# Kernel tuning notes

Measured on AMD Instinct MI355X. Metric: run time of the kernel, lower is better.

Reference implementation:

```python
import jax, jax.numpy as jnp
import numpy as np

B, D, H, DH, L = 2, 1024, 16, 64, 4
FF = 4 * D
COUNTS = (512, 256, 128, 64, 16)  # seq, local_seq, scattering, expression, fusion
EPS = 1e-5


def layer_norm(x, gamma):
    mu = jnp.mean(x, axis=-1, keepdims=True)
    var = jnp.mean((x - mu) ** 2, axis=-1, keepdims=True)
    return (x - mu) * jax.lax.rsqrt(var + EPS) * gamma


def build_zorro_mask(counts):
    # faithful to the torch code, including the `|` / `==` precedence quirk:
    # zorro_mask_fusion = (zorro_mask | tf) == FUSION(4)
    types = jnp.concatenate([jnp.full((c,), i, dtype=jnp.int32) for i, c in enumerate(counts)])
    tf, tt = types[:, None], types[None, :]
    m0 = tf == tt
    fusion_rows = (m0.astype(jnp.int32) | tf) == 4
    mask = m0 | fusion_rows
    S = int(sum(counts))
    nf = counts[4]
    exp_rows = (types == 3)[:, None]
    col_ok = (jnp.arange(S) < (S - nf))[None, :]
    return mask | (exp_rows & col_ok)


def setup_inputs() -> dict:
    key = jax.random.key(0)
    ks = jax.random.split(key, 13)
    s = 0.02
    inp = {
        "rna_tokens": jax.random.normal(ks[0], (B, COUNTS[0], D), jnp.float32),
        "roi_tokens": jax.random.normal(ks[1], (B, COUNTS[1], D), jnp.float32),
        "structure_tokens": jax.random.normal(ks[2], (B, COUNTS[2], D), jnp.float32),
        "expression_tokens": jax.random.normal(ks[3], (B, COUNTS[3], D), jnp.float32),
        "fusion_tokens": jax.random.normal(ks[4], (B, COUNTS[4], D), jnp.float32),
        "qw": jax.random.normal(ks[5], (L, D, H * DH), jnp.float32) * s,
        "kvw": jax.random.normal(ks[6], (L, D, 2 * H * DH), jnp.float32) * s,
        "ow": jax.random.normal(ks[7], (L, H * DH, D), jnp.float32) * s,
        "ag": jnp.ones((L, D), jnp.float32),
        "fg": jnp.ones((L, D), jnp.float32),
        "w1": jax.random.normal(ks[8], (L, D, FF), jnp.float32) * s,
        "w2": jax.random.normal(ks[9], (L, FF, D), jnp.float32) * s,
        "gamma": jnp.ones((D,), jnp.float32),
    }
    return inp


def reference(rna_tokens, roi_tokens, structure_tokens, expression_tokens, fusion_tokens,
              qw, kvw, ow, ag, fg, w1, w2, gamma):
    streams = (rna_tokens, roi_tokens, structure_tokens, expression_tokens, fusion_tokens)
    counts = tuple(t.shape[1] for t in streams)
    tokens = jnp.concatenate(streams, axis=1)  # [B, S, D]
    b, S, d = tokens.shape
    mask = build_zorro_mask(counts)  # [S, S] bool
    scale = DH ** -0.5
    neg = jnp.finfo(tokens.dtype).min
    attn_list = []
    for l in range(L):
        x = layer_norm(tokens, ag[l])
        q = (x @ qw[l]).reshape(b, S, H, DH)
        kv = x @ kvw[l]
        k = kv[..., : H * DH].reshape(b, S, H, DH)
        v = kv[..., H * DH:].reshape(b, S, H, DH)
        sim = jnp.einsum('bihd,bjhd->bhij', q, k) * scale
        sim = jnp.where(mask, sim, neg)
        attn = jax.nn.softmax(sim, axis=-1)  # [B, H, S, S]
        attn_list.append(attn)
        out = jnp.einsum('bhij,bjhd->bihd', attn, v).reshape(b, S, H * DH) @ ow[l]
        tokens = out + tokens
        y = layer_norm(tokens, fg[l])
        tokens = jax.nn.gelu(y @ w1[l], approximate=False) @ w2[l] + tokens
    tokens = layer_norm(tokens, gamma)
    splits = np.cumsum(counts)[:-1].tolist()
    seq_t, local_t, scat_t, exp_t, fus_t = jnp.split(tokens, splits, axis=1)
    return (seq_t, local_t, scat_t, exp_t, fus_t, jnp.stack(attn_list))
```

## Files before the change

### kernel.cpp

```cpp
#include <hip/hip_runtime.h>
#include <math.h>
#include <stdint.h>

typedef __bf16 bf16;
typedef __attribute__((ext_vector_type(8))) bf16 bf16x8;
typedef __attribute__((ext_vector_type(4))) bf16 bf16x4;
typedef __attribute__((ext_vector_type(4))) float f4;

__device__ __forceinline__ f4 mfma(bf16x8 a, bf16x8 b, f4 c){
  return __builtin_amdgcn_mfma_f32_16x16x32_bf16(a, b, c, 0, 0, 0);
}

static constexpr int S_TOT = 976;
static constexpr int MR = 1952;
static constexpr int MRP = 2048;
static constexpr size_t ATT_BASE = 1998848;
static constexpr size_t ATT_L = 30482432;

__device__ __forceinline__ void gload16(const void* g, const void* l){
  __builtin_amdgcn_global_load_lds(
      (const __attribute__((address_space(1))) void*)(uintptr_t)g,
      (__attribute__((address_space(3))) void*)(uint32_t)(uintptr_t)l,
      16, 0, 0);
}

__device__ __forceinline__ unsigned pk2(float a, float b){
  unsigned short ua = __builtin_bit_cast(unsigned short, (bf16)a);
  unsigned short ub = __builtin_bit_cast(unsigned short, (bf16)b);
  return ((unsigned)ub << 16) | (unsigned)ua;
}

__device__ __forceinline__ void mask_span(int r0, int& cs, int& ce){
  if (r0 < 512)      { cs = 0;   ce = 512; }
  else if (r0 < 768) { cs = 512; ce = 768; }
  else if (r0 < 896) { cs = 768; ce = 896; }
  else if (r0 < 960) { cs = 0;   ce = 960; }
  else               { cs = 0;   ce = 976; }
}

__global__ __launch_bounds__(256) void k_zero_mask(float* __restrict__ aout){
  int z = blockIdx.y;
  int r0 = blockIdx.x*16;
  float* base = aout + (size_t)blockIdx.z*ATT_L + (size_t)z*S_TOT*S_TOT;
  int cs, ce; mask_span(r0, cs, ce);
  int cs4 = cs >> 2, ce4 = ce >> 2;
  f4 zf = {0.f,0.f,0.f,0.f};
#pragma unroll
  for (int r2=0;r2<16;r2++){
    f4* rb = (f4*)(base + (size_t)(r0 + r2)*S_TOT);
    for (int c4 = threadIdx.x; c4 < cs4; c4 += 256)        rb[c4] = zf;
    for (int c4 = ce4 + threadIdx.x; c4 < 244; c4 += 256)  rb[c4] = zf;
  }
}

__global__ __launch_bounds__(256) void k_concat_ln(const float* __restrict__ r0, const float* __restrict__ r1,
                                                   const float* __restrict__ r2, const float* __restrict__ r3,
                                                   const float* __restrict__ r4, const float* __restrict__ g,
                                                   float* __restrict__ tok, bf16* __restrict__ xb){
  int wid = threadIdx.x >> 6, lane = threadIdx.x & 63;
  int row = blockIdx.x*4 + wid;
  int b = row / S_TOT, s = row % S_TOT;
  const float* src; int off;
  if (s < 512)      { src = r0; off = b*512 + s; }
  else if (s < 768) { src = r1; off = b*256 + (s-512); }
  else if (s < 896) { src = r2; off = b*128 + (s-768); }
  else if (s < 960) { src = r3; off = b*64  + (s-896); }
  else              { src = r4; off = b*16  + (s-960); }
  const f4* p = (const f4*)src + (size_t)off*256;
  f4 v[4];
  float sum=0.f, sq=0.f;
#pragma unroll
  for (int i=0;i<4;i++){
    v[i] = p[i*64 + lane];
    ((f4*)(tok + (size_t)row*1024))[i*64 + lane] = v[i];
#pragma unroll
    for (int c=0;c<4;c++){ float x=v[i][c]; sum+=x; sq+=x*x; }
  }
#pragma unroll
  for (int d=1; d<64; d<<=1){ sum += __shfl_xor(sum,d); sq += __shfl_xor(sq,d); }
  float mu = sum*(1.f/1024.f);
  float var = sq*(1.f/1024.f) - mu*mu;
  float rs = rsqrtf(var + 1e-5f);
#pragma unroll
  for (int i=0;i<4;i++){
    f4 gg = ((const f4*)g)[i*64 + lane];
    bf16x4 o;
#pragma unroll
    for (int c=0;c<4;c++) o[c] = (bf16)((v[i][c]-mu)*rs*gg[c]);
    *(bf16x4*)&xb[(size_t)row*1024 + (size_t)(i*64+lane)*4] = o;
  }
}

__global__ __launch_bounds__(256) void k_ln_bf(const float* __restrict__ in, const float* __restrict__ g,
                                               bf16* __restrict__ out){
  int wid = threadIdx.x >> 6, lane = threadIdx.x & 63;
  int row = blockIdx.x*4 + wid;
  const float* p = in + (size_t)row*1024;
  f4 v[4];
#pragma unroll
  for (int i=0;i<4;i++) v[i] = ((const f4*)p)[i*64 + lane];
  float sum=0.f, sq=0.f;
#pragma unroll
  for (int i=0;i<4;i++){
#pragma unroll
    for (int c=0;c<4;c++){ float x=v[i][c]; sum+=x; sq+=x*x; } }
#pragma unroll
  for (int d=1; d<64; d<<=1){ sum += __shfl_xor(sum,d); sq += __shfl_xor(sq,d); }
  float mu = sum*(1.f/1024.f);
  float var = sq*(1.f/1024.f) - mu*mu;
  float rs = rsqrtf(var + 1e-5f);
#pragma unroll
  for (int i=0;i<4;i++){
    f4 gg = ((const f4*)g)[i*64 + lane];
    bf16x4 o;
#pragma unroll
    for (int c=0;c<4;c++) o[c] = (bf16)((v[i][c]-mu)*rs*gg[c]);
    *(bf16x4*)&out[(size_t)row*1024 + (size_t)(i*64+lane)*4] = o;
  }
}

template<bool LN>
__global__ __launch_bounds__(256) void k_red_ln(const float* __restrict__ pA, float* __restrict__ tokens,
                                                const float* __restrict__ g, bf16* __restrict__ xb){
  int wid = threadIdx.x >> 6, lane = threadIdx.x & 63;
  int row = blockIdx.x*4 + wid;
  const float* p0 = pA + (size_t)row*1024;
  const float* p1 = pA + (size_t)MRP*1024 + (size_t)row*1024;
  float* tp = tokens + (size_t)row*1024;
  f4 v[4];
  float sum=0.f, sq=0.f;
#pragma unroll
  for (int i=0;i<4;i++){
    f4 a = ((const f4*)p0)[i*64 + lane];
    f4 b = ((const f4*)p1)[i*64 + lane];
    f4 t = ((const f4*)tp)[i*64 + lane];
#pragma unroll
    for (int c=0;c<4;c++){ float x = t[c] + a[c] + b[c]; v[i][c] = x; if (LN){ sum += x; sq += x*x; } }
    ((f4*)tp)[i*64 + lane] = v[i];
  }
  if (LN){
#pragma unroll
    for (int d=1; d<64; d<<=1){ sum += __shfl_xor(sum,d); sq += __shfl_xor(sq,d); }
    float mu = sum*(1.f/1024.f);
    float var = sq*(1.f/1024.f) - mu*mu;
    float rs = rsqrtf(var + 1e-5f);
#pragma unroll
    for (int i=0;i<4;i++){
      f4 gg = ((const f4*)g)[i*64 + lane];
      bf16x4 o;
#pragma unroll
      for (int c=0;c<4;c++) o[c] = (bf16)((v[i][c]-mu)*rs*gg[c]);
      *(bf16x4*)&xb[(size_t)row*1024 + (size_t)(i*64+lane)*4] = o;
    }
  }
}

__global__ __launch_bounds__(256) void k_red_ln_out(const float* __restrict__ pA, float* __restrict__ tokens,
                                                    const float* __restrict__ g, float* __restrict__ out){
  int wid = threadIdx.x >> 6, lane = threadIdx.x & 63;
  int row = blockIdx.x*4 + wid;
  int b = row / S_TOT, s = row % S_TOT;
  size_t dst;
  if (s < 512)      dst = (size_t)(b*512 + s)*1024;
  else if (s < 768) dst = 1048576 + (size_t)(b*256 + (s-512))*1024;
  else if (s < 896) dst = 1572864 + (size_t)(b*128 + (s-768))*1024;
  else if (s < 960) dst = 1835008 + (size_t)(b*64  + (s-896))*1024;
  else              dst = 1966080 + (size_t)(b*16  + (s-960))*1024;
  const float* p0 = pA + (size_t)row*1024;
  const float* p1 = pA + (size_t)MRP*1024 + (size_t)row*1024;
  const float* tp = tokens + (size_t)row*1024;
  f4 v[4];
  float sum=0.f, sq=0.f;
#pragma unroll
  for (int i=0;i<4;i++){
    f4 a = ((const f4*)p0)[i*64 + lane];
    f4 bb = ((const f4*)p1)[i*64 + lane];
    f4 t = ((const f4*)tp)[i*64 + lane];
#pragma unroll
    for (int c=0;c<4;c++){ float x = t[c] + a[c] + bb[c]; v[i][c] = x; sum += x; sq += x*x; }
  }
#pragma unroll
  for (int d=1; d<64; d<<=1){ sum += __shfl_xor(sum,d); sq += __shfl_xor(sq,d); }
  float mu = sum*(1.f/1024.f);
  float var = sq*(1.f/1024.f) - mu*mu;
  float rs = rsqrtf(var + 1e-5f);
#pragma unroll
  for (int i=0;i<4;i++){
    f4 gg = ((const f4*)g)[i*64 + lane];
    f4 o;
#pragma unroll
    for (int c=0;c<4;c++) o[c] = (v[i][c]-mu)*rs*gg[c];
    ((f4*)(out + dst))[i*64 + lane] = o;
  }
}

__global__ __launch_bounds__(256) void k_wtrans_all(const float* __restrict__ qw, const float* __restrict__ kvw,
                                                    const float* __restrict__ ow, const float* __restrict__ w1,
                                                    const float* __restrict__ w2,
                                                    bf16* __restrict__ wqkvT, bf16* __restrict__ woT,
                                                    bf16* __restrict__ w1T, bf16* __restrict__ w2T){
  int t = blockIdx.x;
  int l = t / 12288; t -= l*12288;
  const float* src; bf16* dst; int ldsrc, K, coloff, kb, nb;
  if (t < 3072){
    int c = t >> 10, tt = t & 1023;
    kb = (tt & 31)*32; nb = (tt >> 5)*32;
    if (c == 0){ src = qw + (size_t)l*1048576; ldsrc = 1024; coloff = 0; }
    else       { src = kvw + (size_t)l*2097152; ldsrc = 2048; coloff = (c==2)?1024:0; }
    dst = wqkvT + (size_t)l*3145728 + (size_t)c*1048576; K = 1024;
  } else if (t < 4096){
    int tt = t - 3072;
    kb = (tt & 31)*32; nb = (tt >> 5)*32;
    src = ow + (size_t)l*1048576; ldsrc = 1024; coloff = 0;
    dst = woT + (size_t)l*1048576; K = 1024;
  } else if (t < 8192){
    int tt = t - 4096;
    kb = (tt & 31)*32; nb = (tt >> 5)*32;
    src = w1 + (size_t)l*4194304; ldsrc = 4096; coloff = 0;
    dst = w1T + (size_t)l*4194304; K = 1024;
  } else {
    int tt = t - 8192;
    kb = (tt & 127)*32; nb = (tt >> 7)*32;
    src = w2 + (size_t)l*4194304; ldsrc = 1024; coloff = 0;
    dst = w2T + (size_t)l*4194304; K = 4096;
  }
  __shared__ float tbuf[32][33];
  int tx = threadIdx.x & 31, ty = threadIdx.x >> 5;
#pragma unroll
  for (int i=0;i<32;i+=8) tbuf[ty+i][tx] = src[(size_t)(kb+ty+i)*ldsrc + coloff + nb + tx];
  __syncthreads();
#pragma unroll
  for (int i=0;i<32;i+=8) dst[(size_t)(nb+ty+i)*K + kb + tx] = (bf16)tbuf[tx][ty+i];
}

__global__ __launch_bounds__(256) void k_attn_pv(const bf16* __restrict__ q, const bf16* __restrict__ k,
                                                 const bf16* __restrict__ vT, int ld,
                                                 float* __restrict__ aout, bf16* __restrict__ O){
  int z = blockIdx.y; int b = z >> 4, h = z & 15;
  int wid = threadIdx.x >> 6, lane = threadIdx.x & 63;
  int r0 = (blockIdx.x*4 + wid)*16;
  if (r0 >= S_TOT) return;
  int cs, ce; mask_span(r0, cs, ce);
  int lm = lane & 15, lg = lane >> 4;
  const float scale = 0.125f;
  const bf16* qp = q + (size_t)(b*S_TOT + r0 + lm)*ld + h*64 + lg*8;
  bf16x8 qf0 = *(const bf16x8*)qp;
  bf16x8 qf1 = *(const bf16x8*)(qp + 32);
  const bf16* kbase = k + (size_t)b*S_TOT*ld + h*64 + lg*8;
  const bf16* vbase = vT + (size_t)z*64*S_TOT;
  int nfull = (ce - cs) & ~31;
  bool tail = ((ce - cs) & 16) != 0;
  float s = 0.f;
  for (int cb = cs; cb < cs + nfull; cb += 32){
    const bf16* kp = kbase + (size_t)(cb + lm)*ld;
    bf16x8 k00 = *(const bf16x8*)kp;
    bf16x8 k01 = *(const bf16x8*)(kp + 32);
    const bf16* kp2 = kp + (size_t)16*ld;
    bf16x8 k10 = *(const bf16x8*)kp2;
    bf16x8 k11 = *(const bf16x8*)(kp2 + 32);
    f4 c0 = {0.f,0.f,0.f,0.f}, c1 = {0.f,0.f,0.f,0.f};
    __builtin_amdgcn_s_setprio(1);
    c0 = mfma(k00, qf0, c0); c0 = mfma(k01, qf1, c0);
    c1 = mfma(k10, qf0, c1); c1 = mfma(k11, qf1, c1);
    __builtin_amdgcn_s_setprio(0);
#pragma unroll
    for (int r=0;r<4;r++) s += __expf(c0[r]*scale) + __expf(c1[r]*scale);
  }
  if (tail){
    int cb = cs + nfull;
    const bf16* kp = kbase + (size_t)(cb + lm)*ld;
    bf16x8 k00 = *(const bf16x8*)kp;
    bf16x8 k01 = *(const bf16x8*)(kp + 32);
    f4 c0 = {0.f,0.f,0.f,0.f};
    c0 = mfma(k00, qf0, c0); c0 = mfma(k01, qf1, c0);
#pragma unroll
    for (int r=0;r<4;r++) s += __expf(c0[r]*scale);
  }
  s += __shfl_xor(s, 16);
  s += __shfl_xor(s, 32);
  float inv = 1.f / s;
  float* orow = aout + (size_t)z*S_TOT*S_TOT + (size_t)(r0 + lm)*S_TOT;
  f4 acc[4];
#pragma unroll
  for (int nf=0;nf<4;nf++){ f4 zf = {0.f,0.f,0.f,0.f}; acc[nf] = zf; }
  bool msel = (lg >= 2);
  int srcA = lm + ((lg & 1) << 5);
  int srcB = srcA + 16;
  auto step = [&](int cb, bool has2){
    const bf16* kp = kbase + (size_t)(cb + lm)*ld;
    bf16x8 k00 = *(const bf16x8*)kp;
    bf16x8 k01 = *(const bf16x8*)(kp + 32);
    f4 c0 = {0.f,0.f,0.f,0.f}, c1 = {0.f,0.f,0.f,0.f};
    __builtin_amdgcn_s_setprio(1);
    c0 = mfma(k00, qf0, c0); c0 = mfma(k01, qf1, c0);
    if (has2){
      const bf16* kp2 = kp + (size_t)16*ld;
      bf16x8 k10 = *(const bf16x8*)kp2;
      bf16x8 k11 = *(const bf16x8*)(kp2 + 32);
      c1 = mfma(k10, qf0, c1); c1 = mfma(k11, qf1, c1);
    }
    __builtin_amdgcn_s_setprio(0);
    f4 p0, p1;
#pragma unroll
    for (int r=0;r<4;r++) p0[r] = __expf(c0[r]*scale)*inv;
#pragma unroll
    for (int r=0;r<4;r++) p1[r] = has2 ? __expf(c1[r]*scale)*inv : 0.f;
    *(f4*)(orow + cb + lg*4) = p0;
    if (has2) *(f4*)(orow + cb + 16 + lg*4) = p1;
    unsigned lo0 = pk2(p0[0], p0[1]), hi0 = pk2(p0[2], p0[3]);
    unsigned lo1 = pk2(p1[0], p1[1]), hi1 = pk2(p1[2], p1[3]);
    unsigned a0 = __shfl(lo0, srcA), a1 = __shfl(lo1, srcA);
    unsigned b0 = __shfl(hi0, srcA), b1 = __shfl(hi1, srcA);
    unsigned c0s = __shfl(lo0, srcB), c1s = __shfl(lo1, srcB);
    unsigned d0 = __shfl(hi0, srcB), d1 = __shfl(hi1, srcB);
    union { unsigned u[4]; bf16x8 v; } pu;
    pu.u[0] = msel ? a1 : a0;
    pu.u[1] = msel ? b1 : b0;
    pu.u[2] = msel ? c1s : c0s;
    pu.u[3] = msel ? d1 : d0;
    bf16x8 pa = pu.v;
    __builtin_amdgcn_s_setprio(1);
#pragma unroll
    for (int nf=0;nf<4;nf++){
      bf16x8 vf = *(const bf16x8*)(vbase + (size_t)(nf*16 + lm)*S_TOT + cb + lg*8);
      acc[nf] = mfma(pa, vf, acc[nf]);
    }
    __builtin_amdgcn_s_setprio(0);
  };
  for (int cb = cs; cb < cs + nfull; cb += 32) step(cb, true);
  if (tail) step(cs + nfull, false);
  bf16* obase = O + (size_t)(b*S_TOT + r0)*1024 + h*64;
#pragma unroll
  for (int nf=0;nf<4;nf++)
#pragma unroll
    for (int r=0;r<4;r++)
      obase[(size_t)(lg*4 + r)*1024 + nf*16 + lm] = (bf16)acc[nf][r];
}

template<int BM, bool OUTBF, bool RESID, bool GELU, bool VT>
__global__ __launch_bounds__(256) void k_gemm2(
    const bf16* __restrict__ A, int lda,
    const bf16* __restrict__ Bw, int ldb,
    float* __restrict__ Cf, bf16* __restrict__ Cb, int ldc,
    const float* __restrict__ R, bf16* __restrict__ vTout,
    int M, int N, int K, int kz, long cz)
{
  constexpr int MF = BM/32;
  __shared__ bf16 As[2][BM*32];
  __shared__ bf16 Bs[2][128*32];
  int tid = threadIdx.x, lane = tid & 63, wid = tid >> 6;
  int lm = lane & 15, lg = lane >> 4;
  int wr = (wid >> 1)*(BM/2), wc = (wid & 1)*64;
  int mb = blockIdx.x*BM, nb = blockIdx.y*128;
  int bz = blockIdx.z;
  f4 acc[MF][4];
#pragma unroll
  for (int i=0;i<MF;i++)
#pragma unroll
    for (int j=0;j<4;j++){ f4 zf = {0.f,0.f,0.f,0.f}; acc[i][j] = zf; }
  const bf16* Ab = A + (size_t)mb*lda + (size_t)bz*kz;
  const bf16* Bb = Bw + (size_t)nb*ldb + (size_t)bz*kz;
  auto stage = [&](int kt, int buf){
    int k0 = kt*32;
#pragma unroll
    for (int it=0; it<BM/64; it++){
      int cb = it*256 + wid*64;
      int c  = cb + lane;
      gload16(Ab + (size_t)(c>>2)*lda + k0 + (c&3)*8, (char*)As[buf] + cb*16);
    }
#pragma unroll
    for (int it=0; it<2; it++){
      int cb = it*256 + wid*64;
      int c  = cb + lane;
      gload16(Bb + (size_t)(c>>2)*ldb + k0 + (c&3)*8, (char*)Bs[buf] + cb*16);
    }
  };
  stage(0, 0);
  __syncthreads();
  int nkt = K/32;
  for (int kt=0; kt<nkt; kt++){
    int cur = kt & 1;
    if (kt+1 < nkt) stage(kt+1, cur^1);
    bf16x8 af[MF], bfr[4];
#pragma unroll
    for (int mf=0; mf<MF; mf++) af[mf] = *(bf16x8*)&As[cur][(wr + mf*16 + lm)*32 + lg*8];
#pragma unroll
    for (int nf=0; nf<4; nf++)  bfr[nf] = *(bf16x8*)&Bs[cur][(wc + nf*16 + lm)*32 + lg*8];
#pragma unroll
    for (int mf=0; mf<MF; mf++)
#pragma unroll
      for (int nf=0; nf<4; nf++)
        acc[mf][nf] = mfma(af[mf], bfr[nf], acc[mf][nf]);
    __syncthreads();
  }
#pragma unroll
  for (int mf=0; mf<MF; mf++)
#pragma unroll
    for (int nf=0; nf<4; nf++)
#pragma unroll
      for (int r=0; r<4; r++){
        int row = mb + wr + mf*16 + lg*4 + r;
        if (row < M){
          int col = nb + wc + nf*16 + lm;
          float vv = acc[mf][nf][r];
          if (RESID) vv += R[(size_t)row*ldc + col];
          if (GELU){
            float u2 = vv*(1.5957691216f + 0.0713548162f*vv*vv);
            float e = __expf(u2);
            vv = vv - vv/(e + 1.f);
          }
          if (OUTBF) Cb[(size_t)row*ldc + col] = (bf16)vv;
          else       Cf[(size_t)bz*cz + (size_t)row*ldc + col] = vv;
        }
      }
  if constexpr (VT){
    if (nb >= 2048){
      __shared__ __align__(16) bf16 Ts[128][72];
#pragma unroll
      for (int hb=0; hb<2; hb++){
        __syncthreads();
        if ((wid >> 1) == hb){
#pragma unroll
          for (int mf=0; mf<MF; mf++)
#pragma unroll
            for (int nf=0; nf<4; nf++)
#pragma unroll
              for (int r=0; r<4; r++)
                Ts[wc + nf*16 + lm][mf*16 + lg*4 + r] = (bf16)acc[mf][nf][r];
        }
        __syncthreads();
        int dc = tid >> 1;
        int rh = (tid & 1)*32;
#pragma unroll
        for (int j=0;j<4;j++){
          int lr = rh + j*8;
          int srow = mb + hb*64 + lr;
          if (srow < MR){
            int bb = srow >= S_TOT;
            int ss = srow - bb*S_TOT;
            int gn = nb - 2048 + dc;
            bf16x8 d = *(bf16x8*)&Ts[dc][lr];
            *(bf16x8*)&vTout[((size_t)(bb*16 + (gn>>6))*64 + (gn&63))*S_TOT + ss] = d;
          }
        }
      }
    }
  }
}

extern "C" void kernel_launch(void* const* d_in, const int* in_sizes, int n_in,
                              void* d_out, int out_size, void* d_ws, size_t ws_size,
                              hipStream_t stream) {
  const float* rna  = (const float*)d_in[0];
  const float* roi  = (const float*)d_in[1];
  const float* stru = (const float*)d_in[2];
  const float* expr = (const float*)d_in[3];
  const float* fus  = (const float*)d_in[4];
  const float* qw   = (const float*)d_in[5];
  const float* kvw  = (const float*)d_in[6];
  const float* ow   = (const float*)d_in[7];
  const float* ag   = (const float*)d_in[8];
  const float* fg   = (const float*)d_in[9];
  const float* w1   = (const float*)d_in[10];
  const float* w2   = (const float*)d_in[11];
  const float* gamma= (const float*)d_in[12];
  float* out = (float*)d_out;

  char* wsb = (char*)d_ws;
  size_t off = 0;
  auto alc = [&](size_t n)->char*{ char* p = wsb + off; off = (off + n + 255) & ~(size_t)255; return p; };
  float* tokens = (float*)alc((size_t)MRP*1024*4);
  float* pA    = (float*)alc((size_t)2*MRP*1024*4);
  bf16* xb    = (bf16*)alc((size_t)MRP*1024*2);
  bf16* qkv   = (bf16*)alc((size_t)MRP*3072*2);
  bf16* vT    = (bf16*)alc((size_t)32*64*S_TOT*2);
  bf16* attno = (bf16*)alc((size_t)MRP*1024*2);
  bf16* hb    = (bf16*)alc((size_t)MRP*4096*2);
  bf16* wqkvT = (bf16*)alc((size_t)4*3072*1024*2);
  bf16* woT   = (bf16*)alc((size_t)4*1024*1024*2);
  bf16* w1T   = (bf16*)alc((size_t)4*4096*1024*2);
  bf16* w2T   = (bf16*)alc((size_t)4*4096*1024*2);
  if (off > ws_size) return;

  k_zero_mask<<<dim3(61,32,4), 256, 0, stream>>>(out + ATT_BASE);

  k_wtrans_all<<<4*12288, 256, 0, stream>>>(qw, kvw, ow, w1, w2, wqkvT, woT, w1T, w2T);

  k_concat_ln<<<MR/4, 256, 0, stream>>>(rna, roi, stru, expr, fus, ag, tokens, xb);

  for (int l=0; l<4; l++){
    k_gemm2<128,true,false,false,true><<<dim3(16,24), 256, 0, stream>>>(
        xb, 1024, wqkvT + (size_t)l*3145728, 1024, nullptr, qkv, 3072, nullptr, vT, MR, 3072, 1024, 0, 0);

    float* attL = out + ATT_BASE + (size_t)l*ATT_L;
    k_attn_pv<<<dim3(16,32), 256, 0, stream>>>(qkv, qkv + 1024, vT, 3072, attL, attno);

    k_gemm2<64,false,true,false,false><<<dim3(31,8), 256, 0, stream>>>(
        attno, 1024, woT + (size_t)l*1048576, 1024, tokens, nullptr, 1024, tokens, nullptr, MR, 1024, 1024, 0, 0);

    k_ln_bf<<<MR/4, 256, 0, stream>>>(tokens, fg + l*1024, xb);

    k_gemm2<128,true,false,true,false><<<dim3(16,32), 256, 0, stream>>>(
        xb, 1024, w1T + (size_t)l*4194304, 1024, nullptr, hb, 4096, nullptr, nullptr, MR, 4096, 1024, 0, 0);

    k_gemm2<128,false,false,false,false><<<dim3(16,8,2), 256, 0, stream>>>(
        hb, 4096, w2T + (size_t)l*4194304, 4096, pA, nullptr, 1024, nullptr, nullptr, MR, 1024, 2048,
        2048, (long)MRP*1024);

    if (l < 3) k_red_ln<true><<<MR/4, 256, 0, stream>>>(pA, tokens, ag + (l+1)*1024, xb);
    else       k_red_ln_out<<<MR/4, 256, 0, stream>>>(pA, tokens, gamma, out);
  }
}
```

Baseline: 1.057 ms.

## Cache softmax exponentials in registers and fuse mask zeroing into attention kernel

For query rows whose unmasked key span is at most 512 columns, the attention kernel now computes QK^T and the exponentials once. It keeps them packed as bf16 in registers, then reuses them for the probability write and the PV product, instead of recomputing QK^T in a second pass. Normalisation of the PV accumulator moves to the end. The separate kernel that zeroed the masked regions of the attention output is removed, and each attention wave now zeroes its own rows' masked columns. In exchange the kernel uses many more registers, which may lower occupancy. The stored attention probabilities also go through bf16 rounding before normalisation, which reduces precision.

After: 1.017 ms. 3.8% less time.

```diff
diff --git a/kernel.cpp b/kernel.cpp
--- a/kernel.cpp
+++ b/kernel.cpp
@@ -29,6 +29,8 @@
   unsigned short ub = __builtin_bit_cast(unsigned short, (bf16)b);
   return ((unsigned)ub << 16) | (unsigned)ua;
 }
+__device__ __forceinline__ float ubf_lo(unsigned u){ return __builtin_bit_cast(float, u << 16); }
+__device__ __forceinline__ float ubf_hi(unsigned u){ return __builtin_bit_cast(float, u & 0xffff0000u); }
 
 __device__ __forceinline__ void mask_span(int r0, int& cs, int& ce){
   if (r0 < 512)      { cs = 0;   ce = 512; }
@@ -36,21 +38,6 @@
   else if (r0 < 896) { cs = 768; ce = 896; }
   else if (r0 < 960) { cs = 0;   ce = 960; }
   else               { cs = 0;   ce = 976; }
-}
-
-__global__ __launch_bounds__(256) void k_zero_mask(float* __restrict__ aout){
-  int z = blockIdx.y;
-  int r0 = blockIdx.x*16;
-  float* base = aout + (size_t)blockIdx.z*ATT_L + (size_t)z*S_TOT*S_TOT;
-  int cs, ce; mask_span(r0, cs, ce);
-  int cs4 = cs >> 2, ce4 = ce >> 2;
-  f4 zf = {0.f,0.f,0.f,0.f};
-#pragma unroll
-  for (int r2=0;r2<16;r2++){
-    f4* rb = (f4*)(base + (size_t)(r0 + r2)*S_TOT);
-    for (int c4 = threadIdx.x; c4 < cs4; c4 += 256)        rb[c4] = zf;
-    for (int c4 = ce4 + threadIdx.x; c4 < 244; c4 += 256)  rb[c4] = zf;
-  }
 }
 
 __global__ __launch_bounds__(256) void k_concat_ln(const float* __restrict__ r0, const float* __restrict__ r1,
@@ -248,37 +235,6 @@
   bf16x8 qf1 = *(const bf16x8*)(qp + 32);
   const bf16* kbase = k + (size_t)b*S_TOT*ld + h*64 + lg*8;
   const bf16* vbase = vT + (size_t)z*64*S_TOT;
-  int nfull = (ce - cs) & ~31;
-  bool tail = ((ce - cs) & 16) != 0;
-  float s = 0.f;
-  for (int cb = cs; cb < cs + nfull; cb += 32){
-    const bf16* kp = kbase + (size_t)(cb + lm)*ld;
-    bf16x8 k00 = *(const bf16x8*)kp;
-    bf16x8 k01 = *(const bf16x8*)(kp + 32);
-    const bf16* kp2 = kp + (size_t)16*ld;
-    bf16x8 k10 = *(const bf16x8*)kp2;
-    bf16x8 k11 = *(const bf16x8*)(kp2 + 32);
-    f4 c0 = {0.f,0.f,0.f,0.f}, c1 = {0.f,0.f,0.f,0.f};
-    __builtin_amdgcn_s_setprio(1);
-    c0 = mfma(k00, qf0, c0); c0 = mfma(k01, qf1, c0);
-    c1 = mfma(k10, qf0, c1); c1 = mfma(k11, qf1, c1);
-    __builtin_amdgcn_s_setprio(0);
-#pragma unroll
-    for (int r=0;r<4;r++) s += __expf(c0[r]*scale) + __expf(c1[r]*scale);
-  }
-  if (tail){
-    int cb = cs + nfull;
-    const bf16* kp = kbase + (size_t)(cb + lm)*ld;
-    bf16x8 k00 = *(const bf16x8*)kp;
-    bf16x8 k01 = *(const bf16x8*)(kp + 32);
-    f4 c0 = {0.f,0.f,0.f,0.f};
-    c0 = mfma(k00, qf0, c0); c0 = mfma(k01, qf1, c0);
-#pragma unroll
-    for (int r=0;r<4;r++) s += __expf(c0[r]*scale);
-  }
-  s += __shfl_xor(s, 16);
-  s += __shfl_xor(s, 32);
-  float inv = 1.f / s;
   float* orow = aout + (size_t)z*S_TOT*S_TOT + (size_t)(r0 + lm)*S_TOT;
   f4 acc[4];
 #pragma unroll
@@ -286,55 +242,166 @@
   bool msel = (lg >= 2);
   int srcA = lm + ((lg & 1) << 5);
   int srcB = srcA + 16;
-  auto step = [&](int cb, bool has2){
-    const bf16* kp = kbase + (size_t)(cb + lm)*ld;
-    bf16x8 k00 = *(const bf16x8*)kp;
-    bf16x8 k01 = *(const bf16x8*)(kp + 32);
-    f4 c0 = {0.f,0.f,0.f,0.f}, c1 = {0.f,0.f,0.f,0.f};
-    __builtin_amdgcn_s_setprio(1);
-    c0 = mfma(k00, qf0, c0); c0 = mfma(k01, qf1, c0);
-    if (has2){
+  bf16* obase = O + (size_t)(b*S_TOT + r0)*1024 + h*64;
+
+  if (ce - cs <= 512){
+    constexpr int MAXST = 16;
+    unsigned plo0[MAXST], phi0[MAXST], plo1[MAXST], phi1[MAXST];
+    int nst = (ce - cs) >> 5;
+    float s = 0.f;
+#pragma unroll
+    for (int st=0; st<MAXST; st++){
+      if (st < nst){
+        int cb = cs + st*32;
+        const bf16* kp = kbase + (size_t)(cb + lm)*ld;
+        bf16x8 k00 = *(const bf16x8*)kp;
+        bf16x8 k01 = *(const bf16x8*)(kp + 32);
+        const bf16* kp2 = kp + (size_t)16*ld;
+        bf16x8 k10 = *(const bf16x8*)kp2;
+        bf16x8 k11 = *(const bf16x8*)(kp2 + 32);
+        f4 c0 = {0.f,0.f,0.f,0.f}, c1 = {0.f,0.f,0.f,0.f};
+        __builtin_amdgcn_s_setprio(1);
+        c0 = mfma(k00, qf0, c0); c0 = mfma(k01, qf1, c0);
+        c1 = mfma(k10, qf0, c1); c1 = mfma(k11, qf1, c1);
+        __builtin_amdgcn_s_setprio(0);
+        f4 e0, e1;
+#pragma unroll
+        for (int r=0;r<4;r++){ e0[r] = __expf(c0[r]*scale); e1[r] = __expf(c1[r]*scale); }
+#pragma unroll
+        for (int r=0;r<4;r++) s += e0[r] + e1[r];
+        plo0[st] = pk2(e0[0], e0[1]); phi0[st] = pk2(e0[2], e0[3]);
+        plo1[st] = pk2(e1[0], e1[1]); phi1[st] = pk2(e1[2], e1[3]);
+      }
+    }
+    s += __shfl_xor(s, 16);
+    s += __shfl_xor(s, 32);
+    float inv = 1.f / s;
+#pragma unroll
+    for (int st=0; st<MAXST; st++){
+      if (st < nst){
+        int cb = cs + st*32;
+        f4 p0, p1;
+        p0[0] = ubf_lo(plo0[st])*inv; p0[1] = ubf_hi(plo0[st])*inv;
+        p0[2] = ubf_lo(phi0[st])*inv; p0[3] = ubf_hi(phi0[st])*inv;
+        p1[0] = ubf_lo(plo1[st])*inv; p1[1] = ubf_hi(plo1[st])*inv;
+        p1[2] = ubf_lo(phi1[st])*inv; p1[3] = ubf_hi(phi1[st])*inv;
+        *(f4*)(orow + cb + lg*4) = p0;
+        *(f4*)(orow + cb + 16 + lg*4) = p1;
+        unsigned a0 = __shfl(plo0[st], srcA), a1 = __shfl(plo1[st], srcA);
+        unsigned b0 = __shfl(phi0[st], srcA), b1 = __shfl(phi1[st], srcA);
+        unsigned c0s = __shfl(plo0[st], srcB), c1s = __shfl(plo1[st], srcB);
+        unsigned d0 = __shfl(phi0[st], srcB), d1 = __shfl(phi1[st], srcB);
+        union { unsigned u[4]; bf16x8 v; } pu;
+        pu.u[0] = msel ? a1 : a0;
+        pu.u[1] = msel ? b1 : b0;
+        pu.u[2] = msel ? c1s : c0s;
+        pu.u[3] = msel ? d1 : d0;
+        bf16x8 pa = pu.v;
+        __builtin_amdgcn_s_setprio(1);
+#pragma unroll
+        for (int nf=0;nf<4;nf++){
+          bf16x8 vf = *(const bf16x8*)(vbase + (size_t)(nf*16 + lm)*S_TOT + cb + lg*8);
+          acc[nf] = mfma(pa, vf, acc[nf]);
+        }
+        __builtin_amdgcn_s_setprio(0);
+      }
+    }
+#pragma unroll
+    for (int r=0;r<4;r++){
+      float invq = __shfl(inv, lg*4 + r);
+#pragma unroll
+      for (int nf=0;nf<4;nf++)
+        obase[(size_t)(lg*4 + r)*1024 + nf*16 + lm] = (bf16)(acc[nf][r] * invq);
+    }
+  } else {
+    int nfull = (ce - cs) & ~31;
+    bool tail = ((ce - cs) & 16) != 0;
+    float s = 0.f;
+    for (int cb = cs; cb < cs + nfull; cb += 32){
+      const bf16* kp = kbase + (size_t)(cb + lm)*ld;
+      bf16x8 k00 = *(const bf16x8*)kp;
+      bf16x8 k01 = *(const bf16x8*)(kp + 32);
       const bf16* kp2 = kp + (size_t)16*ld;
       bf16x8 k10 = *(const bf16x8*)kp2;
       bf16x8 k11 = *(const bf16x8*)(kp2 + 32);
+      f4 c0 = {0.f,0.f,0.f,0.f}, c1 = {0.f,0.f,0.f,0.f};
+      __builtin_amdgcn_s_setprio(1);
+      c0 = mfma(k00, qf0, c0); c0 = mfma(k01, qf1, c0);
       c1 = mfma(k10, qf0, c1); c1 = mfma(k11, qf1, c1);
-    }
-    __builtin_amdgcn_s_setprio(0);
-    f4 p0, p1;
-#pragma unroll
-    for (int r=0;r<4;r++) p0[r] = __expf(c0[r]*scale)*inv;
-#pragma unroll
-    for (int r=0;r<4;r++) p1[r] = has2 ? __expf(c1[r]*scale)*inv : 0.f;
-    *(f4*)(orow + cb + lg*4) = p0;
-    if (has2) *(f4*)(orow + cb + 16 + lg*4) = p1;
-    unsigned lo0 = pk2(p0[0], p0[1]), hi0 = pk2(p0[2], p0[3]);
-    unsigned lo1 = pk2(p1[0], p1[1]), hi1 = pk2(p1[2], p1[3]);
-    unsigned a0 = __shfl(lo0, srcA), a1 = __shfl(lo1, srcA);
-    unsigned b0 = __shfl(hi0, srcA), b1 = __shfl(hi1, srcA);
-    unsigned c0s = __shfl(lo0, srcB), c1s = __shfl(lo1, srcB);
-    unsigned d0 = __shfl(hi0, srcB), d1 = __shfl(hi1, srcB);
-    union { unsigned u[4]; bf16x8 v; } pu;
-    pu.u[0] = msel ? a1 : a0;
-    pu.u[1] = msel ? b1 : b0;
-    pu.u[2] = msel ? c1s : c0s;
-    pu.u[3] = msel ? d1 : d0;
-    bf16x8 pa = pu.v;
-    __builtin_amdgcn_s_setprio(1);
-#pragma unroll
-    for (int nf=0;nf<4;nf++){
-      bf16x8 vf = *(const bf16x8*)(vbase + (size_t)(nf*16 + lm)*S_TOT + cb + lg*8);
-      acc[nf] = mfma(pa, vf, acc[nf]);
-    }
-    __builtin_amdgcn_s_setprio(0);
-  };
-  for (int cb = cs; cb < cs + nfull; cb += 32) step(cb, true);
-  if (tail) step(cs + nfull, false);
-  bf16* obase = O + (size_t)(b*S_TOT + r0)*1024 + h*64;
-#pragma unroll
-  for (int nf=0;nf<4;nf++)
-#pragma unroll
-    for (int r=0;r<4;r++)
-      obase[(size_t)(lg*4 + r)*1024 + nf*16 + lm] = (bf16)acc[nf][r];
+      __builtin_amdgcn_s_setprio(0);
+#pragma unroll
+      for (int r=0;r<4;r++) s += __expf(c0[r]*scale) + __expf(c1[r]*scale);
+    }
+    if (tail){
+      int cb = cs + nfull;
+      const bf16* kp = kbase + (size_t)(cb + lm)*ld;
+      bf16x8 k00 = *(const bf16x8*)kp;
+      bf16x8 k01 = *(const bf16x8*)(kp + 32);
+      f4 c0 = {0.f,0.f,0.f,0.f};
+      c0 = mfma(k00, qf0, c0); c0 = mfma(k01, qf1, c0);
+#pragma unroll
+      for (int r=0;r<4;r++) s += __expf(c0[r]*scale);
+    }
+    s += __shfl_xor(s, 16);
+    s += __shfl_xor(s, 32);
+    float inv = 1.f / s;
+    auto step = [&](int cb, bool has2){
+      const bf16* kp = kbase + (size_t)(cb + lm)*ld;
+      bf16x8 k00 = *(const bf16x8*)kp;
+      bf16x8 k01 = *(const bf16x8*)(kp + 32);
+      f4 c0 = {0.f,0.f,0.f,0.f}, c1 = {0.f,0.f,0.f,0.f};
+      __builtin_amdgcn_s_setprio(1);
+      c0 = mfma(k00, qf0, c0); c0 = mfma(k01, qf1, c0);
+      if (has2){
+        const bf16* kp2 = kp + (size_t)16*ld;
+        bf16x8 k10 = *(const bf16x8*)kp2;
+        bf16x8 k11 = *(const bf16x8*)(kp2 + 32);
+        c1 = mfma(k10, qf0, c1); c1 = mfma(k11, qf1, c1);
+      }
+      __builtin_amdgcn_s_setprio(0);
+      f4 p0, p1;
+#pragma unroll
+      for (int r=0;r<4;r++) p0[r] = __expf(c0[r]*scale)*inv;
+#pragma unroll
+      for (int r=0;r<4;r++) p1[r] = has2 ? __expf(c1[r]*scale)*inv : 0.f;
+      *(f4*)(orow + cb + lg*4) = p0;
+      if (has2) *(f4*)(orow + cb + 16 + lg*4) = p1;
+      unsigned lo0 = pk2(p0[0], p0[1]), hi0 = pk2(p0[2], p0[3]);
+      unsigned lo1 = pk2(p1[0], p1[1]), hi1 = pk2(p1[2], p1[3]);
+      unsigned a0 = __shfl(lo0, srcA), a1 = __shfl(lo1, srcA);
+      unsigned b0 = __shfl(hi0, srcA), b1 = __shfl(hi1, srcA);
+      unsigned c0s = __shfl(lo0, srcB), c1s = __shfl(lo1, srcB);
+      unsigned d0 = __shfl(hi0, srcB), d1 = __shfl(hi1, srcB);
+      union { unsigned u[4]; bf16x8 v; } pu;
+      pu.u[0] = msel ? a1 : a0;
+      pu.u[1] = msel ? b1 : b0;
+      pu.u[2] = msel ? c1s : c0s;
+      pu.u[3] = msel ? d1 : d0;
+      bf16x8 pa = pu.v;
+      __builtin_amdgcn_s_setprio(1);
+#pragma unroll
+      for (int nf=0;nf<4;nf++){
+        bf16x8 vf = *(const bf16x8*)(vbase + (size_t)(nf*16 + lm)*S_TOT + cb + lg*8);
+        acc[nf] = mfma(pa, vf, acc[nf]);
+      }
+      __builtin_amdgcn_s_setprio(0);
+    };
+    for (int cb = cs; cb < cs + nfull; cb += 32) step(cb, true);
+    if (tail) step(cs + nfull, false);
+#pragma unroll
+    for (int nf=0;nf<4;nf++)
+#pragma unroll
+      for (int r=0;r<4;r++)
+        obase[(size_t)(lg*4 + r)*1024 + nf*16 + lm] = (bf16)acc[nf][r];
+  }
+  float* zrow = aout + (size_t)z*S_TOT*S_TOT + (size_t)r0*S_TOT;
+  int cs4 = cs >> 2, ce4 = ce >> 2;
+  for (int r2=0;r2<16;r2++){
+    f4* rb = (f4*)(zrow + (size_t)r2*S_TOT);
+    f4 zf = {0.f,0.f,0.f,0.f};
+    for (int c4 = lane; c4 < cs4; c4 += 64)        rb[c4] = zf;
+    for (int c4 = ce4 + lane; c4 < 244; c4 += 64)  rb[c4] = zf;
+  }
 }
 
 template<int BM, bool OUTBF, bool RESID, bool GELU, bool VT>
@@ -482,8 +549,6 @@
   bf16* w2T   = (bf16*)alc((size_t)4*4096*1024*2);
   if (off > ws_size) return;
 
-  k_zero_mask<<<dim3(61,32,4), 256, 0, stream>>>(out + ATT_BASE);
-
   k_wtrans_all<<<4*12288, 256, 0, stream>>>(qw, kvw, ow, w1, w2, wqkvT, woT, w1T, w2T);
 
   k_concat_ln<<<MR/4, 256, 0, stream>>>(rna, roi, stru, expr, fus, ag, tokens, xb);
```
